# Kernel tuning notes

Measured on AMD Instinct MI355X. Metric: run time of the kernel, lower is better.

## Reference

```python
import jax, jax.numpy as jnp
import numpy as np

T, IN, H, OUT, L = 2048, 128, 128, 128, 2


def setup_inputs() -> dict:
    key = jax.random.key(0)
    ks = jax.random.split(key, 12)
    s_in = 1.0 / np.sqrt(IN)
    s_h = 1.0 / np.sqrt(H)
    s_ff = 1.0 / np.sqrt(2 * H)
    return {
        "emb": jax.random.normal(ks[0], (T, IN), jnp.float32),
        "start": jax.random.randint(ks[1], (T,), 0, 2).astype(jnp.int32),
        "w_in": jax.random.normal(ks[2], (H, IN), jnp.float32) * s_in,
        "b_in": jnp.zeros((H,), jnp.float32),
        "w_out": jax.random.normal(ks[3], (OUT, H), jnp.float32) * s_h,
        "b_out": jnp.zeros((OUT,), jnp.float32),
        "w_f": jax.random.normal(ks[4], (L, 1, H), jnp.float32) * s_h,
        "b_f": jnp.zeros((L, 1), jnp.float32),
        "w_i": jax.random.normal(ks[5], (L, 1, H), jnp.float32) * s_h,
        "b_i": jnp.zeros((L, 1), jnp.float32),
        "w_v": jax.random.normal(ks[6], (L, H, H), jnp.float32) * s_h,
        "b_v": jnp.zeros((L, H), jnp.float32),
        "w_q": jax.random.normal(ks[7], (L, H, H), jnp.float32) * s_h,
        "b_q": jnp.zeros((L, H), jnp.float32),
        "w_k": jax.random.normal(ks[8], (L, H, H), jnp.float32) * s_h,
        "b_k": jnp.zeros((L, H), jnp.float32),
        "w_o": jax.random.normal(ks[9], (L, H, H), jnp.float32) * s_h,
        "b_o": jnp.zeros((L, H), jnp.float32),
        "w_ff": jax.random.normal(ks[10], (L, H, 2 * H), jnp.float32) * s_ff,
        "b_ff": jnp.zeros((L, H), jnp.float32),
    }


def _mlstm_layer(x, gate_mask, w_f, b_f, w_i, b_i, w_v, b_v, w_q, b_q, w_k, b_k, w_o, b_o):
    # x: [T, H] layer input; gate_mask: [T] (0.0 at episode starts -> reset)
    Hdim = x.shape[-1]
    i = jnp.exp(x @ w_i.T + b_i)                           # [T, 1] exp input gate
    v = x @ w_v.T + b_v                                    # [T, H]
    k = (x * (1.0 / np.sqrt(Hdim))) @ w_k.T + b_k          # [T, H] (1/sqrt(H) applied before Linear)
    C = i[:, :, None] * (v[:, :, None] * k[:, None, :])    # [T, H, H] gated outer products
    n = i * k                                              # [T, H]
    g = jax.nn.sigmoid(x @ w_f.T + b_f)[:, 0] * gate_mask  # [T] forget gate, zeroed at resets

    def step(carry, inp):
        S, m = carry
        Ct, nt, gt = inp
        S = gt * S + Ct
        m = gt * m + nt
        return (S, m), (S, m)

    init = (jnp.zeros((Hdim, Hdim), x.dtype), jnp.zeros((Hdim,), x.dtype))
    _, (S_all, m_all) = jax.lax.scan(step, init, (C, n, g))  # [T,H,H], [T,H]

    q = x @ w_q.T + b_q                                    # [T, H]
    o = jax.nn.sigmoid(x @ w_o.T + b_o)                    # [T, H]
    num = jnp.einsum('thk,tk->th', S_all, q)               # C @ q per step
    den = jnp.maximum(jnp.abs(jnp.einsum('th,th->t', m_all, q))[:, None], 1.0)
    return o * (num / den)


def reference(emb, start, w_in, b_in, w_out, b_out, w_f, b_f, w_i, b_i,
              w_v, b_v, w_q, b_q, w_k, b_k, w_o, b_o, w_ff, b_ff):
    gate_mask = 1.0 - start.astype(emb.dtype)              # reset => discard previous state
    e = emb @ w_in.T + b_in                                # [T, H]
    z = e
    for l in range(w_f.shape[0]):
        h = _mlstm_layer(z, gate_mask, w_f[l], b_f[l], w_i[l], b_i[l],
                         w_v[l], b_v[l], w_q[l], b_q[l], w_k[l], b_k[l], w_o[l], b_o[l])
        z = jax.nn.leaky_relu(jnp.concatenate([h, e], axis=-1) @ w_ff[l].T + b_ff[l])
    return z @ w_out.T + b_out
```

## Files before the change

kernel.cpp:

```cpp
#include <hip/hip_runtime.h>
#include <math.h>

#define TT 2048
#define HH 128
#define ROWS 8
#define SP 132
#define XR 144
#define NBLK (TT / ROWS)

__device__ __forceinline__ float dot4(float4 a, float4 b) {
    return a.x * b.x + a.y * b.y + a.z * b.z + a.w * b.w;
}

__device__ __forceinline__ int xidx(int r, int k) {
    return r * XR + ((k >> 5) * 36) + (k & 31);
}

__device__ __forceinline__ float2 load_f2_agent(const float* p) {
    unsigned long long u = __hip_atomic_load((const unsigned long long*)p,
                                             __ATOMIC_RELAXED, __HIP_MEMORY_SCOPE_AGENT);
    float2 r;
    r.x = __uint_as_float((unsigned)(u & 0xffffffffull));
    r.y = __uint_as_float((unsigned)(u >> 32));
    return r;
}
__device__ __forceinline__ float load_f_agent(const float* p) {
    return __hip_atomic_load(p, __ATOMIC_RELAXED, __HIP_MEMORY_SCOPE_AGENT);
}
__device__ __forceinline__ void store_f_agent(float* p, float v) {
    __hip_atomic_store(p, v, __ATOMIC_RELAXED, __HIP_MEMORY_SCOPE_AGENT);
}

__global__ __launch_bounds__(256) void prep_kernel(
        const float* __restrict__ w_in, const float* __restrict__ w_out,
        const float* __restrict__ w_v, const float* __restrict__ w_q,
        const float* __restrict__ w_k, const float* __restrict__ w_o,
        const float* __restrict__ w_ff, const int* __restrict__ start,
        float4* __restrict__ win_p, float4* __restrict__ wout_p,
        float4* __restrict__ wcat, float4* __restrict__ wff_p,
        int* __restrict__ stb, unsigned* __restrict__ bar) {
    if (blockIdx.x >= 224) {
        __shared__ int sl[256];
        int base = (blockIdx.x - 224) * 256;
        int t = base + threadIdx.x;
        sl[threadIdx.x] = start[t];
        __syncthreads();
        int s = t;
        while (s > base && sl[s - base] == 0) --s;
        if (s == base && sl[0] == 0) {
            while (s > 0 && start[s] == 0) --s;
        }
        stb[t] = s;
        return;
    }
    int i = blockIdx.x * 256 + threadIdx.x;
    if (blockIdx.x == 0 && threadIdx.x < 16) bar[threadIdx.x] = 0u;
    if (i < 4096) {
        int cg = i >> 7, col = i & 127;
        win_p[i] = ((const float4*)w_in)[col * 32 + cg];
    } else if (i < 8192) {
        int j = i - 4096, cg = j >> 7, col = j & 127;
        wout_p[j] = ((const float4*)w_out)[col * 32 + cg];
    } else if (i < 40960) {
        int j = i - 8192;
        int l = j >> 14, r = j & 16383, cg = r >> 9, col = r & 511;
        int sel = col >> 7, cm = col & 127;
        const float* s = (sel == 0 ? w_v : sel == 1 ? w_q : sel == 2 ? w_k : w_o) + l * HH * HH;
        wcat[j] = ((const float4*)s)[cm * 32 + cg];
    } else {
        int j = i - 40960;
        int l = j >> 13, r = j & 8191, cg = r >> 7, col = r & 127;
        const float* s = w_ff + l * HH * 256;
        wff_p[j] = ((const float4*)s)[col * 64 + cg];
    }
}

__device__ __forceinline__ void grid_barrier(unsigned* __restrict__ ctr) {
    __syncthreads();
    if (threadIdx.x == 0) {
        atomicAdd(ctr, 1u);
        while (__hip_atomic_load(ctr, __ATOMIC_RELAXED, __HIP_MEMORY_SCOPE_AGENT)
               < (unsigned)NBLK) {
            __builtin_amdgcn_s_sleep(8);
        }
    }
    __syncthreads();
}

__device__ __forceinline__ void attn_row(int t0,
        const float* __restrict__ kb, const float* __restrict__ vb,
        const float* __restrict__ qs, const float* __restrict__ os,
        const float* __restrict__ g, const float* __restrict__ iexp,
        const int* __restrict__ stb, float* __restrict__ hs) {
    int tid = threadIdx.x;
    int wv = tid >> 6, lane = tid & 63;
    int t = t0 + wv;
    int st = stb[t];
    float2 q2 = *(const float2*)(qs + wv * SP + 2 * lane);
    float2 o2 = *(const float2*)(os + wv * SP + 2 * lane);
    float nx = 0.f, ny = 0.f, dsum = 0.f, decay = 1.f;
    int tp = t;
    while (tp >= st) {
        int nb = tp - st + 1; if (nb > 4) nb = 4;
        float2 kk[4], vv[4];
        float ie[4], gv[4];
#pragma unroll
        for (int b = 0; b < 4; ++b) {
            if (b < nb) {
                kk[b] = load_f2_agent(kb + (tp - b) * HH + 2 * lane);
                vv[b] = load_f2_agent(vb + (tp - b) * HH + 2 * lane);
                ie[b] = load_f_agent(iexp + (tp - b));
                gv[b] = load_f_agent(g + (tp - b));
            }
        }
#pragma unroll
        for (int b = 0; b < 4; ++b) {
            if (b < nb) {
                float p = kk[b].x * q2.x + kk[b].y * q2.y;
#pragma unroll
                for (int off = 1; off <= 32; off <<= 1) p += __shfl_xor(p, off, 64);
                float coeff = decay * ie[b] * p;
                nx += coeff * vv[b].x; ny += coeff * vv[b].y; dsum += coeff;
                if (tp - b > st) decay *= gv[b];
            }
        }
        tp -= nb;
    }
    float inv = 1.f / fmaxf(fabsf(dsum), 1.f);
    int d = 2 * lane;
    *(float2*)(hs + wv * XR + (d >> 5) * 36 + (d & 31)) =
        make_float2(o2.x * nx * inv, o2.y * ny * inv);
}

__device__ __forceinline__ void proj_fi(int t0, const float* __restrict__ xls,
        const float* __restrict__ w_f, const float* __restrict__ b_f,
        const float* __restrict__ w_i, const float* __restrict__ b_i,
        const int* __restrict__ start, float* __restrict__ g, float* __restrict__ iexp) {
    int tid = threadIdx.x;
    int wv = tid >> 6, lane = tid & 63;
    if (wv >= 8) return;
    int d = 2 * lane;
    float2 xv = *(const float2*)(xls + wv * XR + (d >> 5) * 36 + (d & 31));
    float pf = xv.x * w_f[d] + xv.y * w_f[d + 1];
    float pi = xv.x * w_i[d] + xv.y * w_i[d + 1];
#pragma unroll
    for (int off = 1; off <= 32; off <<= 1) {
        pf += __shfl_xor(pf, off, 64);
        pi += __shfl_xor(pi, off, 64);
    }
    if (lane == 0) {
        int t = t0 + wv;
        store_f_agent(g + t, start[t] ? 0.f : 1.f / (1.f + expf(-(pf + b_f[0]))));
        store_f_agent(iexp + t, expf(pi + b_i[0]));
    }
}

__device__ __forceinline__ void proj_block(int t0, const float* __restrict__ xls,
        const float4* __restrict__ wc,
        const float* __restrict__ b_v, const float* __restrict__ b_q,
        const float* __restrict__ b_k, const float* __restrict__ b_o,
        float* __restrict__ kb, float* __restrict__ vb,
        float* __restrict__ qs, float* __restrict__ os) {
    int tid = threadIdx.x;
    int lane = tid & 63, w = tid >> 6;
    int kc = lane >> 4, c = lane & 15;
    int cslot = (w & 7) * 16 + c;
    int mp = w >> 3;
    float a0[8] = {}, a1[8] = {};
#pragma unroll
    for (int j = 0; j < 8; ++j) {
        const float4* wb = wc + (kc * 8 + j) * 512 + mp * 256;
        float4 w0 = wb[cslot];
        float4 w1 = wb[128 + cslot];
#pragma unroll
        for (int rr = 0; rr < 8; ++rr) {
            float4 x4 = *(const float4*)(xls + rr * XR + kc * 36 + 4 * j);
            a0[rr] += dot4(x4, w0);
            a1[rr] += dot4(x4, w1);
        }
    }
#pragma unroll
    for (int rr = 0; rr < 8; ++rr) {
        a0[rr] += __shfl_xor(a0[rr], 16, 64); a0[rr] += __shfl_xor(a0[rr], 32, 64);
        a1[rr] += __shfl_xor(a1[rr], 16, 64); a1[rr] += __shfl_xor(a1[rr], 32, 64);
    }
    if (kc == 0) {
        if (mp == 0) {
            float bv = b_v[cslot], bq = b_q[cslot];
#pragma unroll
            for (int rr = 0; rr < 8; ++rr) {
                store_f_agent(vb + (t0 + rr) * HH + cslot, a0[rr] + bv);
                qs[rr * SP + cslot] = a1[rr] + bq;
            }
        } else {
            const float ks = 0.088388347648318447f;
            float bk = b_k[cslot], bo = b_o[cslot];
#pragma unroll
            for (int rr = 0; rr < 8; ++rr) {
                store_f_agent(kb + (t0 + rr) * HH + cslot, a0[rr] * ks + bk);
                os[rr * SP + cslot] = 1.f / (1.f + expf(-(a1[rr] + bo)));
            }
        }
    }
}

__device__ __forceinline__ void ffe_block(const float* __restrict__ esb,
        const float4* __restrict__ wffg, float* __restrict__ zp) {
    int tid = threadIdx.x;
    int lane = tid & 63, w = tid >> 6;
    int kc = lane >> 4, c = lane & 15;
    int cslot = (w - 8) * 16 + c;
    float acc[8] = {};
#pragma unroll
    for (int j = 0; j < 8; ++j) {
        float4 w0 = wffg[(32 + kc * 8 + j) * 128 + cslot];
#pragma unroll
        for (int rr = 0; rr < 8; ++rr) {
            float4 x4 = *(const float4*)(esb + rr * XR + kc * 36 + 4 * j);
            acc[rr] += dot4(x4, w0);
        }
    }
#pragma unroll
    for (int rr = 0; rr < 8; ++rr) {
        acc[rr] += __shfl_xor(acc[rr], 16, 64);
        acc[rr] += __shfl_xor(acc[rr], 32, 64);
    }
    if (kc == 0) {
#pragma unroll
        for (int rr = 0; rr < 8; ++rr) zp[rr * SP + cslot] = acc[rr];
    }
}

__device__ __forceinline__ void ffh_block(const float* __restrict__ hsb,
        const float4* wshl, const float* __restrict__ zp,
        const float* __restrict__ b_ff, float* __restrict__ zs) {
    int tid = threadIdx.x;
    int lane = tid & 63, w = tid >> 6;
    int kc = lane >> 4, c = lane & 15;
    int rg = w >> 3;
    int cslot = (w & 7) * 16 + c;
    float acc[4] = {};
#pragma unroll
    for (int j = 0; j < 8; ++j) {
        float4 w0 = wshl[(kc * 8 + j) * 128 + cslot];
#pragma unroll
        for (int rr = 0; rr < 4; ++rr) {
            float4 x4 = *(const float4*)(hsb + (rg * 4 + rr) * XR + kc * 36 + 4 * j);
            acc[rr] += dot4(x4, w0);
        }
    }
#pragma unroll
    for (int rr = 0; rr < 4; ++rr) {
        acc[rr] += __shfl_xor(acc[rr], 16, 64);
        acc[rr] += __shfl_xor(acc[rr], 32, 64);
    }
    if (kc == 0) {
        float bb = b_ff[cslot];
#pragma unroll
        for (int rr = 0; rr < 4; ++rr) {
            int r = rg * 4 + rr;
            float z = acc[rr] + zp[r * SP + cslot] + bb;
            z = z > 0.f ? z : 0.01f * z;
            zs[xidx(r, cslot)] = z;
        }
    }
}

__device__ __forceinline__ void dense128(int t0, const float* __restrict__ xls,
        const float4* __restrict__ Wp, const float* __restrict__ b,
        float* __restrict__ yg, float* __restrict__ ys) {
    int tid = threadIdx.x;
    int lane = tid & 63, w = tid >> 6;
    int kc = lane >> 3, c = lane & 7;
    int col = (w >> 3) * 64 + (w & 7) * 8 + c;
    float a0[8] = {};
#pragma unroll
    for (int j = 0; j < 4; ++j) {
        float4 w0 = Wp[(kc * 4 + j) * 128 + col];
        int off = (kc >> 1) * 36 + (kc & 1) * 16 + 4 * j;
#pragma unroll
        for (int rr = 0; rr < 8; ++rr) {
            float4 x4 = *(const float4*)(xls + rr * XR + off);
            a0[rr] += dot4(x4, w0);
        }
    }
#pragma unroll
    for (int rr = 0; rr < 8; ++rr) {
        a0[rr] += __shfl_xor(a0[rr], 8, 64);
        a0[rr] += __shfl_xor(a0[rr], 16, 64);
        a0[rr] += __shfl_xor(a0[rr], 32, 64);
    }
    if (kc == 0) {
        float bb = b[col];
#pragma unroll
        for (int rr = 0; rr < 8; ++rr) {
            float y = a0[rr] + bb;
            if (ys) ys[xidx(rr, col)] = y;
            if (yg) yg[(t0 + rr) * HH + col] = y;
        }
    }
}

__device__ __forceinline__ void stage_wsh_h(const float4* __restrict__ src, float4* lds) {
    int tid2 = threadIdx.x - 512;
    int wv2 = tid2 >> 6;
#pragma unroll
    for (int it = 0; it < 8; ++it) {
        __builtin_amdgcn_global_load_lds(
            (const __attribute__((address_space(1))) unsigned int*)(src + it * 512 + tid2),
            (__attribute__((address_space(3))) unsigned int*)(lds + it * 512 + wv2 * 64),
            16, 0, 0);
    }
}

__global__ __launch_bounds__(1024, 4) void mega_kernel(
        const float* __restrict__ emb, const int* __restrict__ start,
        const float4* __restrict__ win_p, const float* __restrict__ b_in,
        const float4* __restrict__ wcat,
        const float* __restrict__ b_v, const float* __restrict__ b_q,
        const float* __restrict__ b_k, const float* __restrict__ b_o,
        const float* __restrict__ w_f, const float* __restrict__ b_f,
        const float* __restrict__ w_i, const float* __restrict__ b_i,
        const float4* __restrict__ wff_p, const float* __restrict__ b_ff,
        const float4* __restrict__ wout_p, const float* __restrict__ b_out,
        float* __restrict__ k0b, float* __restrict__ v0b,
        float* __restrict__ k1b, float* __restrict__ v1b,
        float* __restrict__ g0, float* __restrict__ i0,
        float* __restrict__ g1, float* __restrict__ i1,
        const int* __restrict__ stb, unsigned* __restrict__ bar,
        float* __restrict__ out) {
    __shared__ float xs[ROWS * XR];
    __shared__ float es[ROWS * XR];
    __shared__ float hs[ROWS * XR];
    __shared__ float zs[ROWS * XR];
    __shared__ float qs[ROWS * SP];
    __shared__ float os[ROWS * SP];
    __shared__ float zp[ROWS * SP];
    __shared__ float4 wsh[4096];
    int tid = threadIdx.x;
    int t0 = blockIdx.x * ROWS;
    int wv = tid >> 6;

    {
        int row = tid >> 7, dd = tid & 127;
        xs[row * XR + (dd >> 5) * 36 + (dd & 31)] = emb[(t0 + row) * HH + dd];
    }
    __syncthreads();
    dense128(t0, xs, win_p, b_in, (float*)0, es);
    __syncthreads();
    proj_block(t0, es, wcat, b_v, b_q, b_k, b_o, k0b, v0b, qs, os);
    proj_fi(t0, es, w_f, b_f, w_i, b_i, start, g0, i0);
    grid_barrier(bar + 0);

    if (wv < 8) {
        attn_row(t0, k0b, v0b, qs, os, g0, i0, stb, hs);
    } else {
        stage_wsh_h(wff_p, wsh);
        ffe_block(es, wff_p, zp);
    }
    __syncthreads();
    ffh_block(hs, wsh, zp, b_ff, zs);
    __syncthreads();
    proj_block(t0, zs, wcat + 16384, b_v + HH, b_q + HH, b_k + HH, b_o + HH,
               k1b, v1b, qs, os);
    proj_fi(t0, zs, w_f + HH, b_f + 1, w_i + HH, b_i + 1, start, g1, i1);
    grid_barrier(bar + 1);

    if (wv < 8) {
        attn_row(t0, k1b, v1b, qs, os, g1, i1, stb, hs);
    } else {
        stage_wsh_h(wff_p + 8192, wsh);
        ffe_block(es, wff_p + 8192, zp);
    }
    __syncthreads();
    ffh_block(hs, wsh, zp, b_ff + HH, zs);
    __syncthreads();
    dense128(t0, zs, wout_p, b_out, out, (float*)0);
}

extern "C" void kernel_launch(void* const* d_in, const int* in_sizes, int n_in,
                              void* d_out, int out_size, void* d_ws, size_t ws_size,
                              hipStream_t stream) {
    const float* emb   = (const float*)d_in[0];
    const int*   start = (const int*)  d_in[1];
    const float* w_in  = (const float*)d_in[2];
    const float* b_in  = (const float*)d_in[3];
    const float* w_out = (const float*)d_in[4];
    const float* b_out = (const float*)d_in[5];
    const float* w_f   = (const float*)d_in[6];
    const float* b_f   = (const float*)d_in[7];
    const float* w_i   = (const float*)d_in[8];
    const float* b_i   = (const float*)d_in[9];
    const float* w_v   = (const float*)d_in[10];
    const float* b_v   = (const float*)d_in[11];
    const float* w_q   = (const float*)d_in[12];
    const float* b_q   = (const float*)d_in[13];
    const float* w_k   = (const float*)d_in[14];
    const float* b_k   = (const float*)d_in[15];
    const float* w_o   = (const float*)d_in[16];
    const float* b_o   = (const float*)d_in[17];
    const float* w_ff  = (const float*)d_in[18];
    const float* b_ff  = (const float*)d_in[19];
    float* out = (float*)d_out;

    unsigned* bar = (unsigned*)d_ws;
    float* ws = (float*)d_ws + 64;
    float* k0b = ws; ws += TT * HH;
    float* v0b = ws; ws += TT * HH;
    float* k1b = ws; ws += TT * HH;
    float* v1b = ws; ws += TT * HH;
    float* g0  = ws; ws += TT;
    float* i0  = ws; ws += TT;
    float* g1  = ws; ws += TT;
    float* i1  = ws; ws += TT;
    int* stb   = (int*)ws; ws += TT;
    float4* win_p  = (float4*)ws; ws += 16384;
    float4* wout_p = (float4*)ws; ws += 16384;
    float4* wcat   = (float4*)ws; ws += 131072;
    float4* wff_p  = (float4*)ws; ws += 65536;

    prep_kernel<<<dim3(232), dim3(256), 0, stream>>>(
        w_in, w_out, w_v, w_q, w_k, w_o, w_ff, start,
        win_p, wout_p, wcat, wff_p, stb, bar);
    mega_kernel<<<dim3(NBLK), dim3(1024), 0, stream>>>(
        emb, start, win_p, b_in, wcat,
        b_v, b_q, b_k, b_o, w_f, b_f, w_i, b_i,
        wff_p, b_ff, wout_p, b_out,
        k0b, v0b, k1b, v1b, g0, i0, g1, i1,
        stb, bar, out);
}
```

Measured before the change: 138.0 us.

## Replace grid barriers with per-block ready flags and local in-block attention

```diff
diff --git a/kernel.cpp b/kernel.cpp
--- a/kernel.cpp
+++ b/kernel.cpp
@@ -30,6 +30,9 @@
 __device__ __forceinline__ void store_f_agent(float* p, float v) {
     __hip_atomic_store(p, v, __ATOMIC_RELAXED, __HIP_MEMORY_SCOPE_AGENT);
 }
+__device__ __forceinline__ unsigned load_u_agent(const unsigned* p) {
+    return __hip_atomic_load(p, __ATOMIC_RELAXED, __HIP_MEMORY_SCOPE_AGENT);
+}
 
 __global__ __launch_bounds__(256) void prep_kernel(
         const float* __restrict__ w_in, const float* __restrict__ w_out,
@@ -38,7 +41,7 @@
         const float* __restrict__ w_ff, const int* __restrict__ start,
         float4* __restrict__ win_p, float4* __restrict__ wout_p,
         float4* __restrict__ wcat, float4* __restrict__ wff_p,
-        int* __restrict__ stb, unsigned* __restrict__ bar) {
+        int* __restrict__ stb, unsigned* __restrict__ flags) {
     if (blockIdx.x >= 224) {
         __shared__ int sl[256];
         int base = (blockIdx.x - 224) * 256;
@@ -53,8 +56,8 @@
         stb[t] = s;
         return;
     }
+    if (blockIdx.x == 0) flags[threadIdx.x] = 0u;
     int i = blockIdx.x * 256 + threadIdx.x;
-    if (blockIdx.x == 0 && threadIdx.x < 16) bar[threadIdx.x] = 0u;
     if (i < 4096) {
         int cg = i >> 7, col = i & 127;
         win_p[i] = ((const float4*)w_in)[col * 32 + cg];
@@ -75,22 +78,13 @@
     }
 }
 
-__device__ __forceinline__ void grid_barrier(unsigned* __restrict__ ctr) {
-    __syncthreads();
-    if (threadIdx.x == 0) {
-        atomicAdd(ctr, 1u);
-        while (__hip_atomic_load(ctr, __ATOMIC_RELAXED, __HIP_MEMORY_SCOPE_AGENT)
-               < (unsigned)NBLK) {
-            __builtin_amdgcn_s_sleep(8);
-        }
-    }
-    __syncthreads();
-}
-
-__device__ __forceinline__ void attn_row(int t0,
+__device__ __forceinline__ void attn_row(int t0, int bid, unsigned phase,
+        const unsigned* __restrict__ flags,
         const float* __restrict__ kb, const float* __restrict__ vb,
+        const float* __restrict__ kl, const float* __restrict__ vl,
         const float* __restrict__ qs, const float* __restrict__ os,
         const float* __restrict__ g, const float* __restrict__ iexp,
+        const float* __restrict__ gl, const float* __restrict__ il,
         const int* __restrict__ stb, float* __restrict__ hs) {
     int tid = threadIdx.x;
     int wv = tid >> 6, lane = tid & 63;
@@ -99,32 +93,49 @@
     float2 q2 = *(const float2*)(qs + wv * SP + 2 * lane);
     float2 o2 = *(const float2*)(os + wv * SP + 2 * lane);
     float nx = 0.f, ny = 0.f, dsum = 0.f, decay = 1.f;
-    int tp = t;
-    while (tp >= st) {
-        int nb = tp - st + 1; if (nb > 4) nb = 4;
-        float2 kk[4], vv[4];
-        float ie[4], gv[4];
-#pragma unroll
-        for (int b = 0; b < 4; ++b) {
-            if (b < nb) {
-                kk[b] = load_f2_agent(kb + (tp - b) * HH + 2 * lane);
-                vv[b] = load_f2_agent(vb + (tp - b) * HH + 2 * lane);
-                ie[b] = load_f_agent(iexp + (tp - b));
-                gv[b] = load_f_agent(g + (tp - b));
+    int lo = st > t0 ? st : t0;
+    for (int tp = t; tp >= lo; --tp) {
+        int r = tp - t0;
+        float2 k2 = *(const float2*)(kl + r * SP + 2 * lane);
+        float2 v2 = *(const float2*)(vl + r * SP + 2 * lane);
+        float p = k2.x * q2.x + k2.y * q2.y;
+#pragma unroll
+        for (int off = 1; off <= 32; off <<= 1) p += __shfl_xor(p, off, 64);
+        float coeff = decay * il[r] * p;
+        nx += coeff * v2.x; ny += coeff * v2.y; dsum += coeff;
+        if (tp > st) decay *= gl[r];
+    }
+    if (st < t0) {
+        for (int j = st >> 3; j < bid; ++j) {
+            while (load_u_agent(flags + j) < phase) __builtin_amdgcn_s_sleep(1);
+        }
+        int tp = t0 - 1;
+        while (tp >= st) {
+            int nb = tp - st + 1; if (nb > 4) nb = 4;
+            float2 kk[4], vv[4];
+            float ie[4], gv[4];
+#pragma unroll
+            for (int b = 0; b < 4; ++b) {
+                if (b < nb) {
+                    kk[b] = load_f2_agent(kb + (tp - b) * HH + 2 * lane);
+                    vv[b] = load_f2_agent(vb + (tp - b) * HH + 2 * lane);
+                    ie[b] = load_f_agent(iexp + (tp - b));
+                    gv[b] = load_f_agent(g + (tp - b));
+                }
             }
-        }
-#pragma unroll
-        for (int b = 0; b < 4; ++b) {
-            if (b < nb) {
-                float p = kk[b].x * q2.x + kk[b].y * q2.y;
-#pragma unroll
-                for (int off = 1; off <= 32; off <<= 1) p += __shfl_xor(p, off, 64);
-                float coeff = decay * ie[b] * p;
-                nx += coeff * vv[b].x; ny += coeff * vv[b].y; dsum += coeff;
-                if (tp - b > st) decay *= gv[b];
+#pragma unroll
+            for (int b = 0; b < 4; ++b) {
+                if (b < nb) {
+                    float p = kk[b].x * q2.x + kk[b].y * q2.y;
+#pragma unroll
+                    for (int off = 1; off <= 32; off <<= 1) p += __shfl_xor(p, off, 64);
+                    float coeff = decay * ie[b] * p;
+                    nx += coeff * vv[b].x; ny += coeff * vv[b].y; dsum += coeff;
+                    if (tp - b > st) decay *= gv[b];
+                }
             }
-        }
-        tp -= nb;
+            tp -= nb;
+        }
     }
     float inv = 1.f / fmaxf(fabsf(dsum), 1.f);
     int d = 2 * lane;
@@ -135,7 +146,8 @@
 __device__ __forceinline__ void proj_fi(int t0, const float* __restrict__ xls,
         const float* __restrict__ w_f, const float* __restrict__ b_f,
         const float* __restrict__ w_i, const float* __restrict__ b_i,
-        const int* __restrict__ start, float* __restrict__ g, float* __restrict__ iexp) {
+        const int* __restrict__ start, float* __restrict__ g, float* __restrict__ iexp,
+        float* __restrict__ gl, float* __restrict__ il) {
     int tid = threadIdx.x;
     int wv = tid >> 6, lane = tid & 63;
     if (wv >= 8) return;
@@ -150,8 +162,12 @@
     }
     if (lane == 0) {
         int t = t0 + wv;
-        store_f_agent(g + t, start[t] ? 0.f : 1.f / (1.f + expf(-(pf + b_f[0]))));
-        store_f_agent(iexp + t, expf(pi + b_i[0]));
+        float gvv = start[t] ? 0.f : 1.f / (1.f + expf(-(pf + b_f[0])));
+        float ivv = expf(pi + b_i[0]);
+        store_f_agent(g + t, gvv);
+        store_f_agent(iexp + t, ivv);
+        gl[wv] = gvv;
+        il[wv] = ivv;
     }
 }
 
@@ -160,6 +176,7 @@
         const float* __restrict__ b_v, const float* __restrict__ b_q,
         const float* __restrict__ b_k, const float* __restrict__ b_o,
         float* __restrict__ kb, float* __restrict__ vb,
+        float* __restrict__ kl, float* __restrict__ vl,
         float* __restrict__ qs, float* __restrict__ os) {
     int tid = threadIdx.x;
     int lane = tid & 63, w = tid >> 6;
@@ -189,7 +206,9 @@
             float bv = b_v[cslot], bq = b_q[cslot];
 #pragma unroll
             for (int rr = 0; rr < 8; ++rr) {
-                store_f_agent(vb + (t0 + rr) * HH + cslot, a0[rr] + bv);
+                float vv = a0[rr] + bv;
+                store_f_agent(vb + (t0 + rr) * HH + cslot, vv);
+                vl[rr * SP + cslot] = vv;
                 qs[rr * SP + cslot] = a1[rr] + bq;
             }
         } else {
@@ -197,7 +216,9 @@
             float bk = b_k[cslot], bo = b_o[cslot];
 #pragma unroll
             for (int rr = 0; rr < 8; ++rr) {
-                store_f_agent(kb + (t0 + rr) * HH + cslot, a0[rr] * ks + bk);
+                float kk = a0[rr] * ks + bk;
+                store_f_agent(kb + (t0 + rr) * HH + cslot, kk);
+                kl[rr * SP + cslot] = kk;
                 os[rr * SP + cslot] = 1.f / (1.f + expf(-(a1[rr] + bo)));
             }
         }
@@ -327,7 +348,7 @@
         float* __restrict__ k1b, float* __restrict__ v1b,
         float* __restrict__ g0, float* __restrict__ i0,
         float* __restrict__ g1, float* __restrict__ i1,
-        const int* __restrict__ stb, unsigned* __restrict__ bar,
+        const int* __restrict__ stb, unsigned* __restrict__ flags,
         float* __restrict__ out) {
     __shared__ float xs[ROWS * XR];
     __shared__ float es[ROWS * XR];
@@ -336,9 +357,13 @@
     __shared__ float qs[ROWS * SP];
     __shared__ float os[ROWS * SP];
     __shared__ float zp[ROWS * SP];
+    __shared__ float kl[ROWS * SP];
+    __shared__ float vl[ROWS * SP];
+    __shared__ float gl[ROWS], il[ROWS];
     __shared__ float4 wsh[4096];
     int tid = threadIdx.x;
-    int t0 = blockIdx.x * ROWS;
+    int bid = blockIdx.x;
+    int t0 = bid * ROWS;
     int wv = tid >> 6;
 
     {
@@ -348,12 +373,14 @@
     __syncthreads();
     dense128(t0, xs, win_p, b_in, (float*)0, es);
     __syncthreads();
-    proj_block(t0, es, wcat, b_v, b_q, b_k, b_o, k0b, v0b, qs, os);
-    proj_fi(t0, es, w_f, b_f, w_i, b_i, start, g0, i0);
-    grid_barrier(bar + 0);
+    proj_block(t0, es, wcat, b_v, b_q, b_k, b_o, k0b, v0b, kl, vl, qs, os);
+    proj_fi(t0, es, w_f, b_f, w_i, b_i, start, g0, i0, gl, il);
+    __syncthreads();
+    if (tid == 0)
+        __hip_atomic_store(flags + bid, 1u, __ATOMIC_RELAXED, __HIP_MEMORY_SCOPE_AGENT);
 
     if (wv < 8) {
-        attn_row(t0, k0b, v0b, qs, os, g0, i0, stb, hs);
+        attn_row(t0, bid, 1u, flags, k0b, v0b, kl, vl, qs, os, g0, i0, gl, il, stb, hs);
     } else {
         stage_wsh_h(wff_p, wsh);
         ffe_block(es, wff_p, zp);
@@ -362,12 +389,14 @@
     ffh_block(hs, wsh, zp, b_ff, zs);
     __syncthreads();
     proj_block(t0, zs, wcat + 16384, b_v + HH, b_q + HH, b_k + HH, b_o + HH,
-               k1b, v1b, qs, os);
-    proj_fi(t0, zs, w_f + HH, b_f + 1, w_i + HH, b_i + 1, start, g1, i1);
-    grid_barrier(bar + 1);
+               k1b, v1b, kl, vl, qs, os);
+    proj_fi(t0, zs, w_f + HH, b_f + 1, w_i + HH, b_i + 1, start, g1, i1, gl, il);
+    __syncthreads();
+    if (tid == 0)
+        __hip_atomic_store(flags + bid, 2u, __ATOMIC_RELAXED, __HIP_MEMORY_SCOPE_AGENT);
 
     if (wv < 8) {
-        attn_row(t0, k1b, v1b, qs, os, g1, i1, stb, hs);
+        attn_row(t0, bid, 2u, flags, k1b, v1b, kl, vl, qs, os, g1, i1, gl, il, stb, hs);
     } else {
         stage_wsh_h(wff_p + 8192, wsh);
         ffe_block(es, wff_p + 8192, zp);
@@ -403,8 +432,8 @@
     const float* b_ff  = (const float*)d_in[19];
     float* out = (float*)d_out;
 
-    unsigned* bar = (unsigned*)d_ws;
-    float* ws = (float*)d_ws + 64;
+    unsigned* flags = (unsigned*)d_ws;
+    float* ws = (float*)d_ws + 256;
     float* k0b = ws; ws += TT * HH;
     float* v0b = ws; ws += TT * HH;
     float* k1b = ws; ws += TT * HH;
@@ -421,11 +450,11 @@
 
     prep_kernel<<<dim3(232), dim3(256), 0, stream>>>(
         w_in, w_out, w_v, w_q, w_k, w_o, w_ff, start,
-        win_p, wout_p, wcat, wff_p, stb, bar);
+        win_p, wout_p, wcat, wff_p, stb, flags);
     mega_kernel<<<dim3(NBLK), dim3(1024), 0, stream>>>(
         emb, start, win_p, b_in, wcat,
         b_v, b_q, b_k, b_o, w_f, b_f, w_i, b_i,
         wff_p, b_ff, wout_p, b_out,
         k0b, v0b, k1b, v1b, g0, i0, g1, i1,
-        stb, bar, out);
-}
+        stb, flags, out);
+}
```

New measurement: 125.2 us. 1.1x faster.
